# Kernel optimization log

Measured on AMD Instinct MI355X. Metric: run time of the kernel, lower is better.

Reference implementation:

```python
import jax, jax.numpy as jnp
import numpy as np

K = 4
TEMP = 34.0
KS = 3
PAD = 1
STRIDE = 1


def setup_inputs() -> dict:
    key = jax.random.key(0)
    k0, k1, k2, k3, k4, k5 = jax.random.split(key, 6)
    B, C, H, W = 32, 256, 56, 56
    OC = 256
    HID = int(C * 0.25) + 1  # 65
    x = jax.random.normal(k0, (B, C, H, W), jnp.float32)
    # kaiming-ish scales for the 1x1 attention convs (treated as matmuls)
    w_fc1 = jax.random.normal(k1, (HID, C), jnp.float32) * np.float32(np.sqrt(2.0 / C))
    w_fc2 = jax.random.normal(k2, (K, HID), jnp.float32) * np.float32(np.sqrt(2.0 / HID))
    b_fc2 = jnp.zeros((K,), jnp.float32)
    # positive step sizes for numerical sanity (torch inits randn then overwrites at init_state)
    alpha = jax.random.uniform(k3, (K, 1), jnp.float32, minval=0.05, maxval=1.0)
    weight = jax.random.normal(k4, (K, OC, C, KS, KS), jnp.float32) * 0.05
    bias_w = jax.random.normal(k5, (K, OC), jnp.float32) * 0.01
    return dict(x=x, w_fc1=w_fc1, w_fc2=w_fc2, b_fc2=b_fc2, alpha=alpha,
                weight=weight, bias_w=bias_w)


def _round_ste(v):
    # round_pass: forward round, backward identity
    return v + jax.lax.stop_gradient(jnp.round(v) - v)


def _lsq_quant(w2d, alpha):
    # Faithful to the torch LSQQuantizer forward (eval path): divide by per-row
    # alpha, clamp ONLY scalar elements [0,0],[1,0],[2,0] (as the torch code does),
    # then straight-through round and rescale. grad_scale copies into .data and
    # therefore has no effect on values or the autograd graph.
    d = w2d / alpha  # (K, M)
    d = d.at[0, 0].set(jnp.clip(d[0, 0], -2.0, 1.0))   # 2-bit range
    d = d.at[1, 0].set(jnp.clip(d[1, 0], -4.0, 3.0))   # 3-bit range
    d = d.at[2, 0].set(jnp.clip(d[2, 0], -8.0, 7.0))   # 4-bit range
    return _round_ste(d) * alpha


def reference(x, w_fc1, w_fc2, b_fc2, alpha, weight, bias_w):
    B, C, H, W = x.shape
    Kk, OC = bias_w.shape
    # attention2d: global avg pool -> 1x1 conv -> relu -> 1x1 conv (+bias)
    pooled = x.mean(axis=(2, 3))                     # (B, C)
    h = jax.nn.relu(pooled @ w_fc1.T)                # (B, HID)
    raw = h @ w_fc2.T + b_fc2                        # (B, K)
    # gradient_approximation: forward = one-hot(argmax), backward = softmax(x/T)
    soft = jax.nn.softmax(raw / TEMP, axis=1)
    hard = jax.nn.one_hot(jnp.argmax(raw, axis=1), Kk, dtype=raw.dtype)
    attn = soft + jax.lax.stop_gradient(hard - soft)  # (B, K)
    # LSQ-quantize flattened expert weights, then per-sample aggregation
    wq = _lsq_quant(weight.reshape(Kk, -1), alpha)   # (K, OC*C*KS*KS)
    agg_w = (attn @ wq).reshape(B, OC, C, KS, KS)    # per-sample kernels
    agg_b = attn @ bias_w                            # (B, OC)
    # per-sample conv2d (equivalent to the groups=batch trick)
    def conv1(xb, wb):
        return jax.lax.conv_general_dilated(
            xb[None], wb, (STRIDE, STRIDE), [(PAD, PAD), (PAD, PAD)],
            dimension_numbers=('NCHW', 'OIHW', 'NCHW'))[0]
    out = jax.vmap(conv1)(x, agg_w) + agg_b[:, :, None, None]  # (B, OC, H, W)
    return (out, raw)
```

## Files before the change

### kernel.cpp

```cpp
#include <hip/hip_runtime.h>
#include <hip/hip_bf16.h>

typedef __attribute__((ext_vector_type(8))) short short8;
typedef __attribute__((ext_vector_type(16))) float f32x16;

#define XPAD_OFF   0u
#define WQ_OFF     55115776u
#define POOL_OFF   59834368u
#define IDX_OFF    59867136u

__device__ __forceinline__ void gl_lds16(const void* g, void* l) {
  __builtin_amdgcn_global_load_lds(
      (const __attribute__((address_space(1))) unsigned int*)g,
      (__attribute__((address_space(3))) unsigned int*)l, 16, 0, 0);
}

__global__ __launch_bounds__(128) void fc_argmax_kernel(
    const float* __restrict__ pooled, const float* __restrict__ w_fc1,
    const float* __restrict__ w_fc2, const float* __restrict__ b_fc2,
    float* __restrict__ raw_out, int* __restrict__ idx) {
  __shared__ float h[65];
  __shared__ float raws[4];
  const int b = blockIdx.x, t = threadIdx.x;
  if (t < 65) {
    float s = 0.f;
    const float* pb = pooled + b * 256;
    const float* wr = w_fc1 + t * 256;
    for (int c = 0; c < 256; ++c) s += pb[c] * wr[c];
    s *= (1.0f / 3136.0f);
    h[t] = s > 0.f ? s : 0.f;
  }
  __syncthreads();
  if (t < 4) {
    float s = b_fc2[t];
    const float* wr = w_fc2 + t * 65;
    for (int j = 0; j < 65; ++j) s += h[j] * wr[j];
    raws[t] = s;
    raw_out[b * 4 + t] = s;
  }
  __syncthreads();
  if (t == 0) {
    int best = 0; float bv = raws[0];
    for (int k = 1; k < 4; ++k) if (raws[k] > bv) { bv = raws[k]; best = k; }
    idx[b] = best;
  }
}

__global__ __launch_bounds__(256) void quant_kernel(
    const float* __restrict__ weight, const float* __restrict__ alpha,
    __hip_bfloat16* __restrict__ Wq) {
  const unsigned d = blockIdx.x * 256u + threadIdx.x;
  const unsigned cl   = d & 7u;
  const unsigned g    = d >> 3;
  const unsigned lane = g & 63u;
  const unsigned u    = g >> 6;
  const unsigned low  = u & 63u;
  const unsigned s      = low & 1u;
  const unsigned octile = (low >> 1) & 1u;
  const unsigned wm     = (low >> 2) & 1u;
  const unsigned cbh    = (low >> 3) & 7u;
  const unsigned t6   = u >> 6;
  const unsigned tap  = t6 % 9u;
  const unsigned q    = t6 / 9u;
  const unsigned ot   = q & 1u;
  const unsigned k    = q >> 1;
  const unsigned oc = ot * 128u + wm * 64u + octile * 32u + (lane & 31u);
  const unsigned ch = cbh * 32u + s * 16u + (lane >> 5) * 8u + cl;
  const float a = alpha[k];
  float v = weight[(size_t)k * 589824u + oc * 2304u + ch * 9u + tap] / a;
  if (oc == 0u && ch == 0u && tap == 0u) {
    if (k == 0u)      v = fminf(fmaxf(v, -2.f), 1.f);
    else if (k == 1u) v = fminf(fmaxf(v, -4.f), 3.f);
    else if (k == 2u) v = fminf(fmaxf(v, -8.f), 7.f);
  }
  Wq[d] = __float2bfloat16(rintf(v) * a);
}

__global__ __launch_bounds__(256) void padx_kernel(const float* __restrict__ x,
                                                   __hip_bfloat16* __restrict__ Xpad,
                                                   float* __restrict__ pooled) {
  __shared__ float T[56 * 133];
  const int yp = blockIdx.x;
  const int c0 = blockIdx.y * 128;
  const int b  = blockIdx.z;
  const int tid = threadIdx.x;
  __hip_bfloat16* orow = Xpad + ((size_t)(b * 58 + yp) * 58) * 256 + c0;
  const short8 zero8 = (short8){0, 0, 0, 0, 0, 0, 0, 0};
  const bool rowin = (yp >= 1 && yp <= 56);
  if (rowin) {
    const float4* xb4 = (const float4*)(x + (((size_t)b * 256 + c0) * 56 + (yp - 1)) * 56);
    for (int i = tid; i < 1792; i += 256) {
      const int cl = i / 14, p4 = i - cl * 14;
      const float4 v = xb4[(size_t)cl * 784 + p4];
      float* Tp = &T[(p4 * 4) * 133 + cl];
      Tp[0] = v.x; Tp[133] = v.y; Tp[266] = v.z; Tp[399] = v.w;
    }
    __syncthreads();
    if (tid < 128) {
      float s = 0.f;
      for (int px = 0; px < 56; ++px) s += T[px * 133 + tid];
      atomicAdd(pooled + b * 256 + c0 + tid, s);
    }
    for (int i = tid; i < 896; i += 256) {
      const int px = i >> 4, cg = (i & 15) * 8;
      union { short8 v; __hip_bfloat16 e[8]; } u;
      #pragma unroll
      for (int r = 0; r < 8; ++r) u.e[r] = __float2bfloat16(T[px * 133 + cg + r]);
      *(short8*)&orow[(px + 1) * 256 + cg] = u.v;
    }
    for (int i = tid; i < 32; i += 256) {
      const int cg = (i & 15) * 8;
      const int xp = (i >> 4) ? 57 : 0;
      *(short8*)&orow[xp * 256 + cg] = zero8;
    }
  } else {
    for (int i = tid; i < 58 * 16; i += 256) {
      const int xp = i >> 4, cg = (i & 15) * 8;
      *(short8*)&orow[xp * 256 + cg] = zero8;
    }
  }
}

__global__ __launch_bounds__(256, 2) void conv_kernel(
    const __hip_bfloat16* __restrict__ Xpad, const __hip_bfloat16* __restrict__ Wq,
    const int* __restrict__ idx, const float* __restrict__ bias_w,
    float* __restrict__ out) {
  __shared__ __attribute__((aligned(16))) __hip_bfloat16 Xs[22784];

  const int tid = threadIdx.x;
  const int lane = tid & 63;
  const int w = tid >> 6;
  const int wm = w & 1;
  const int wn = w >> 1;

  const int b  = blockIdx.x;
  const int pt = blockIdx.y >> 1;
  const int ot = blockIdx.y & 1;
  const int Y0 = pt * 4;
  const int OC0 = ot * 128;
  const int kb = idx[b];

  const __hip_bfloat16* xb = Xpad + (size_t)b * (58 * 58 * 256);
  const short8* W0 = (const short8*)Wq + (size_t)(kb * 2 + ot) * 36864;

  f32x16 acc[2][4];
  #pragma unroll
  for (int i = 0; i < 2; ++i)
    #pragma unroll
    for (int j = 0; j < 4; ++j)
      acc[i][j] = (f32x16){0,0,0,0,0,0,0,0,0,0,0,0,0,0,0,0};

  const int nlo = lane & 31;
  const int khalf = lane >> 5;

  auto stageseg = [&](int cbn, int bufsel, int k) {
    int sidx = k * 64 + lane;
    int p = sidx >> 2;
    if (p > 347) p = 347;
    const int gsel = (sidx & 3) ^ ((p >> 1) & 3);
    const int r = p / 58, xc = p - r * 58;
    gl_lds16(xb + (((Y0 + r) * 58 + xc) * 256 + cbn * 32 + gsel * 8),
             (char*)Xs + bufsel * 22784 + k * 1024);
  };

  for (int k = w; k < 22; k += 4) stageseg(0, 0, k);
  __syncthreads();

  short8 afr[3][4];
  #pragma unroll
  for (int oc2 = 0; oc2 < 2; ++oc2)
    #pragma unroll
    for (int s2 = 0; s2 < 2; ++s2) {
      afr[0][oc2 * 2 + s2] = W0[0 * 4096 + 0 * 512 + wm * 256 + oc2 * 128 + s2 * 64 + lane];
      afr[1][oc2 * 2 + s2] = W0[1 * 4096 + 0 * 512 + wm * 256 + oc2 * 128 + s2 * 64 + lane];
    }

  for (int cbh = 0; cbh < 8; ++cbh) {
    const __hip_bfloat16* cur = Xs + (cbh & 1) * 11392;
    const int nb = (cbh + 1) & 1;

    #pragma unroll
    for (int t = 0; t < 9; ++t) {
      const int dy = t / 3, dx = t - dy * 3;
      if (cbh < 7) {
        if (t < 5) stageseg(cbh + 1, nb, w + 4 * t);
        else if (t == 5 && w < 2) stageseg(cbh + 1, nb, w + 20);
      }
      if (cbh < 7 || t < 7) {
        const int tap2 = (t + 2) % 9, cb2 = cbh + (t + 2) / 9;
        #pragma unroll
        for (int oc2 = 0; oc2 < 2; ++oc2)
          #pragma unroll
          for (int s2 = 0; s2 < 2; ++s2)
            afr[(t + 2) % 3][oc2 * 2 + s2] =
                W0[tap2 * 4096 + cb2 * 512 + wm * 256 + oc2 * 128 + s2 * 64 + lane];
      }
      #pragma unroll
      for (int s = 0; s < 2; ++s) {
        #pragma unroll
        for (int j = 0; j < 4; ++j) {
          const int row = wn * 2 + (j >> 1) + dy;
          const int col = (j & 1) * 32 + nlo + dx;
          const int p = row * 58 + col;
          const int slot = p * 4 + ((s * 2 + khalf) ^ ((p >> 1) & 3));
          const short8 bfr = *(const short8*)&cur[slot * 8];
          #pragma unroll
          for (int i = 0; i < 2; ++i)
            acc[i][j] = __builtin_amdgcn_mfma_f32_32x32x16_bf16(
                afr[t % 3][i * 2 + s], bfr, acc[i][j], 0, 0, 0);
        }
      }
    }
    __syncthreads();
  }

  const float* biasb = bias_w + kb * 256;
  #pragma unroll
  for (int i = 0; i < 2; ++i) {
    #pragma unroll
    for (int j = 0; j < 4; ++j) {
      const int xcol = (j & 1) * 32 + nlo;
      if (xcol < 56) {
        const int y = Y0 + wn * 2 + (j >> 1);
        #pragma unroll
        for (int reg = 0; reg < 16; ++reg) {
          const int row = (reg & 3) + 8 * (reg >> 2) + 4 * khalf;
          const int oc = OC0 + wm * 64 + i * 32 + row;
          out[(((size_t)b * 256 + oc) * 56 + y) * 56 + xcol] =
              acc[i][j][reg] + biasb[oc];
        }
      }
    }
  }
}

extern "C" void kernel_launch(void* const* d_in, const int* in_sizes, int n_in,
                              void* d_out, int out_size, void* d_ws, size_t ws_size,
                              hipStream_t stream) {
  const float* x      = (const float*)d_in[0];
  const float* w_fc1  = (const float*)d_in[1];
  const float* w_fc2  = (const float*)d_in[2];
  const float* b_fc2  = (const float*)d_in[3];
  const float* alpha  = (const float*)d_in[4];
  const float* weight = (const float*)d_in[5];
  const float* bias_w = (const float*)d_in[6];

  float* out = (float*)d_out;
  float* raw_out = out + (size_t)32 * 256 * 56 * 56;

  char* ws = (char*)d_ws;
  __hip_bfloat16* Xpad = (__hip_bfloat16*)(ws + XPAD_OFF);
  __hip_bfloat16* Wq   = (__hip_bfloat16*)(ws + WQ_OFF);
  float* pooled        = (float*)(ws + POOL_OFF);
  int* idx             = (int*)(ws + IDX_OFF);

  hipMemsetAsync(pooled, 0, 32 * 256 * sizeof(float), stream);
  padx_kernel<<<dim3(58, 2, 32), 256, 0, stream>>>(x, Xpad, pooled);
  quant_kernel<<<9216, 256, 0, stream>>>(weight, alpha, Wq);
  fc_argmax_kernel<<<32, 128, 0, stream>>>(pooled, w_fc1, w_fc2, b_fc2, raw_out, idx);
  conv_kernel<<<dim3(32, 28), 256, 0, stream>>>(Xpad, Wq, idx, bias_w, out);
}
```

Baseline: 330.9 us.

## Coalesce weight quantization through LDS staging and fold pooled zeroing into it

The quant kernel now loads contiguous float4 rows of the expert weights into shared memory and then emits the MFMA-friendly bf16 layout with 16-byte stores, replacing the old strided per-element gather. Block 0 of the quant kernel zeroes the pooled buffer, which removes the separate memset launch, and quant now runs before padx. The fc kernel's dot product also uses float4 loads. The gain depends on how much of the total time quant accounts for compared with the conv kernel, and the pooled zeroing now relies on the two kernels executing in stream order.

New measurement: 328.5 us, median of 2. No clear change (-0.7%).

```diff
diff --git a/kernel.cpp b/kernel.cpp
--- a/kernel.cpp
+++ b/kernel.cpp
@@ -24,9 +24,12 @@
   const int b = blockIdx.x, t = threadIdx.x;
   if (t < 65) {
     float s = 0.f;
-    const float* pb = pooled + b * 256;
-    const float* wr = w_fc1 + t * 256;
-    for (int c = 0; c < 256; ++c) s += pb[c] * wr[c];
+    const float4* pb = (const float4*)(pooled + b * 256);
+    const float4* wr = (const float4*)(w_fc1 + t * 256);
+    for (int c = 0; c < 64; ++c) {
+      const float4 a4 = pb[c], b4 = wr[c];
+      s += a4.x * b4.x + a4.y * b4.y + a4.z * b4.z + a4.w * b4.w;
+    }
     s *= (1.0f / 3136.0f);
     h[t] = s > 0.f ? s : 0.f;
   }
@@ -48,32 +51,56 @@
 
 __global__ __launch_bounds__(256) void quant_kernel(
     const float* __restrict__ weight, const float* __restrict__ alpha,
-    __hip_bfloat16* __restrict__ Wq) {
-  const unsigned d = blockIdx.x * 256u + threadIdx.x;
-  const unsigned cl   = d & 7u;
-  const unsigned g    = d >> 3;
-  const unsigned lane = g & 63u;
-  const unsigned u    = g >> 6;
-  const unsigned low  = u & 63u;
-  const unsigned s      = low & 1u;
-  const unsigned octile = (low >> 1) & 1u;
-  const unsigned wm     = (low >> 2) & 1u;
-  const unsigned cbh    = (low >> 3) & 7u;
-  const unsigned t6   = u >> 6;
-  const unsigned tap  = t6 % 9u;
-  const unsigned q    = t6 / 9u;
-  const unsigned ot   = q & 1u;
-  const unsigned k    = q >> 1;
-  const unsigned oc = ot * 128u + wm * 64u + octile * 32u + (lane & 31u);
-  const unsigned ch = cbh * 32u + s * 16u + (lane >> 5) * 8u + cl;
+    __hip_bfloat16* __restrict__ Wq, float* __restrict__ pooled) {
+  __shared__ __attribute__((aligned(16))) float Ws[32 * 292];
+  const int tid = threadIdx.x;
+  const int B = blockIdx.x;
+  if (B == 0) {
+    for (int i = tid; i < 8192; i += 256) pooled[i] = 0.f;
+  }
+  const int cbh    = B & 7;
+  const int octile = (B >> 3) & 1;
+  const int wm     = (B >> 4) & 1;
+  const int ot     = (B >> 5) & 1;
+  const int k      = B >> 6;
+  const int oc0 = ot * 128 + wm * 64 + octile * 32;
+
+  const int ocr = tid >> 3, q = tid & 7;
+  const float4* src = (const float4*)weight +
+                      (size_t)k * 147456 + (size_t)(oc0 + ocr) * 576 + cbh * 72;
+  #pragma unroll
+  for (int j = 0; j < 9; ++j) {
+    const float4 v = src[q + 8 * j];
+    *(float4*)&Ws[ocr * 292 + 4 * (q + 8 * j)] = v;
+  }
+  __syncthreads();
+
+  const int p    = tid >> 7;
+  const int s    = (tid >> 6) & 1;
+  const int lane = tid & 63;
+  const int ocl  = lane & 31;
+  const int khl  = lane >> 5;
   const float a = alpha[k];
-  float v = weight[(size_t)k * 589824u + oc * 2304u + ch * 9u + tap] / a;
-  if (oc == 0u && ch == 0u && tap == 0u) {
-    if (k == 0u)      v = fminf(fmaxf(v, -2.f), 1.f);
-    else if (k == 1u) v = fminf(fmaxf(v, -4.f), 3.f);
-    else if (k == 2u) v = fminf(fmaxf(v, -8.f), 7.f);
-  }
-  Wq[d] = __float2bfloat16(rintf(v) * a);
+  const int ubase = ((k * 2 + ot) * 9) * 64 + (cbh * 8 + wm * 4 + octile * 2 + s);
+  #pragma unroll
+  for (int m = 0; m < 5; ++m) {
+    const int tap = 2 * m + p;
+    if (tap > 8) break;
+    union { short8 v; __hip_bfloat16 e[8]; } uo;
+    #pragma unroll
+    for (int cl = 0; cl < 8; ++cl) {
+      const int chl = s * 16 + khl * 8 + cl;
+      float v = Ws[ocl * 292 + chl * 9 + tap] / a;
+      if (oc0 == 0 && ocl == 0 && cbh == 0 && chl == 0 && tap == 0) {
+        if (k == 0)      v = fminf(fmaxf(v, -2.f), 1.f);
+        else if (k == 1) v = fminf(fmaxf(v, -4.f), 3.f);
+        else if (k == 2) v = fminf(fmaxf(v, -8.f), 7.f);
+      }
+      uo.e[cl] = __float2bfloat16(rintf(v) * a);
+    }
+    const size_t u = (size_t)(ubase + tap * 64);
+    *(short8*)&Wq[u * 512 + lane * 8] = uo.v;
+  }
 }
 
 __global__ __launch_bounds__(256) void padx_kernel(const float* __restrict__ x,
@@ -254,9 +281,8 @@
   float* pooled        = (float*)(ws + POOL_OFF);
   int* idx             = (int*)(ws + IDX_OFF);
 
-  hipMemsetAsync(pooled, 0, 32 * 256 * sizeof(float), stream);
+  quant_kernel<<<256, 256, 0, stream>>>(weight, alpha, Wq, pooled);
   padx_kernel<<<dim3(58, 2, 32), 256, 0, stream>>>(x, Xpad, pooled);
-  quant_kernel<<<9216, 256, 0, stream>>>(weight, alpha, Wq);
   fc_argmax_kernel<<<32, 128, 0, stream>>>(pooled, w_fc1, w_fc2, b_fc2, raw_out, idx);
   conv_kernel<<<dim3(32, 28), 256, 0, stream>>>(Xpad, Wq, idx, bias_w, out);
 }
```
